# Kernel tuning notes

Hardware: AMD Instinct MI355X
Metric: run time of the kernel (lower is better)

Reference implementation:

```python
import jax, jax.numpy as jnp
import numpy as np

D_MODEL = 2048
N_HEAD = 16
HEAD_DIM = D_MODEL // N_HEAD
SCALE = 1.0 / (HEAD_DIM ** 0.5)


def setup_inputs() -> dict:
    key = jax.random.key(0)
    kx, kq, kk, kv, ko = jax.random.split(key, 5)
    std = 1.0 / np.sqrt(D_MODEL)
    return {
        "x": jax.random.normal(kx, (2, 2048, D_MODEL), dtype=jnp.float32),
        "w_q": jax.random.normal(kq, (D_MODEL, D_MODEL), dtype=jnp.float32) * std,
        "w_k": jax.random.normal(kk, (D_MODEL, D_MODEL), dtype=jnp.float32) * std,
        "w_v": jax.random.normal(kv, (D_MODEL, D_MODEL), dtype=jnp.float32) * std,
        "w_o": jax.random.normal(ko, (D_MODEL, D_MODEL), dtype=jnp.float32) * std,
    }


def reference(x, w_q, w_k, w_v, w_o):
    b, s, d = x.shape
    # nn.Linear(d,d,bias=False): y = x @ W^T, weights stored [out, in]
    def proj(w):
        y = jnp.einsum("bsd,ed->bse", x, w)
        return y.reshape(b, s, N_HEAD, HEAD_DIM).transpose(0, 2, 1, 3)  # [b,h,s,hd]
    q, k, v = proj(w_q), proj(w_k), proj(w_v)
    scores = jnp.einsum("bhqd,bhkd->bhqk", q, k) * SCALE  # [b,h,s,s]
    probs = jax.nn.softmax(scores, axis=-1)
    attn = jnp.einsum("bhqk,bhkd->bhqd", probs, v)
    attn = attn.transpose(0, 2, 1, 3).reshape(b, s, d)
    return jnp.einsum("bsd,ed->bse", attn, w_o)
```

## Files before the change

### kernel.cpp

```cpp
#include <hip/hip_runtime.h>

#define D_MODEL 2048
#define SEQ 2048
#define BATCH 2
#define NH 16
#define HD 128
#define MTOT (BATCH * SEQ)

static constexpr float SCALE_LOG2E = 0.08838834764831845f * 1.4426950408889634f;

typedef __bf16 bf16x8 __attribute__((ext_vector_type(8)));
typedef _Float16 f16x4 __attribute__((ext_vector_type(4)));
typedef float f32x4 __attribute__((ext_vector_type(4)));

__device__ inline unsigned short f2bf(float f) {
  unsigned int u = __builtin_bit_cast(unsigned int, f);
  u += 0x7fffu + ((u >> 16) & 1u);
  return (unsigned short)(u >> 16);
}

__device__ inline float fast_exp2(float x) {
#if __has_builtin(__builtin_amdgcn_exp2f)
  return __builtin_amdgcn_exp2f(x);
#else
  return exp2f(x);
#endif
}

__device__ inline void gload_lds16(const void* g, void* s) {
  __builtin_amdgcn_global_load_lds(
      (__attribute__((address_space(1))) void*)g,
      (__attribute__((address_space(3))) void*)s, 16, 0, 0);
}

__global__ __launch_bounds__(256) void cvt_bf16(const float* __restrict__ in,
                                                unsigned short* __restrict__ out,
                                                int n4) {
  int i = blockIdx.x * 256 + threadIdx.x;
  if (i < n4) {
    float4 v = ((const float4*)in)[i];
    ushort4 o;
    o.x = f2bf(v.x); o.y = f2bf(v.y); o.z = f2bf(v.z); o.w = f2bf(v.w);
    ((ushort4*)out)[i] = o;
  }
}

template <int OUT_BF16>
__global__ __launch_bounds__(256, 2) void gemm_bt(
    const unsigned short* __restrict__ A, const unsigned short* __restrict__ B,
    void* __restrict__ Cp, int M, int N, int K) {
  __shared__ __align__(16) unsigned short As[128 * 32];
  __shared__ __align__(16) unsigned short Bs[128 * 32];
  const int tid = threadIdx.x;
  const int lane = tid & 63;
  const int wave = tid >> 6;
  const int m0 = blockIdx.y * 128;
  const int n0 = blockIdx.x * 128;
  const int wm = (wave >> 1) * 64;
  const int wn = (wave & 1) * 64;

  const int c0 = wave * 2, c1 = wave * 2 + 1;
  const int sr0 = c0 * 16 + (lane >> 2);
  const int sr1 = c1 * 16 + (lane >> 2);
  const int sk = (lane & 3) * 8;
  const unsigned short* Ag0 = A + (size_t)(m0 + sr0) * K + sk;
  const unsigned short* Ag1 = A + (size_t)(m0 + sr1) * K + sk;
  const unsigned short* Bg0 = B + (size_t)(n0 + sr0) * K + sk;
  const unsigned short* Bg1 = B + (size_t)(n0 + sr1) * K + sk;
  unsigned short* lA0 = As + c0 * 512;
  unsigned short* lA1 = As + c1 * 512;
  unsigned short* lB0 = Bs + c0 * 512;
  unsigned short* lB1 = Bs + c1 * 512;

  f32x4 acc[4][4] = {};
  const int fm = lane & 15;
  const int fk = (lane >> 4) * 8;

  for (int k0 = 0; k0 < K; k0 += 32) {
    __syncthreads();
    gload_lds16(Ag0 + k0, lA0);
    gload_lds16(Ag1 + k0, lA1);
    gload_lds16(Bg0 + k0, lB0);
    gload_lds16(Bg1 + k0, lB1);
    __builtin_amdgcn_s_waitcnt(0);
    __syncthreads();
    bf16x8 a[4], b[4];
#pragma unroll
    for (int i = 0; i < 4; i++)
      a[i] = *(const bf16x8*)(As + (wm + i * 16 + fm) * 32 + fk);
#pragma unroll
    for (int j = 0; j < 4; j++)
      b[j] = *(const bf16x8*)(Bs + (wn + j * 16 + fm) * 32 + fk);
#pragma unroll
    for (int i = 0; i < 4; i++)
#pragma unroll
      for (int j = 0; j < 4; j++)
        acc[i][j] = __builtin_amdgcn_mfma_f32_16x16x32_bf16(a[i], b[j], acc[i][j], 0, 0, 0);
  }

  const int er = (lane >> 4) * 4;
  const int ec = lane & 15;
#pragma unroll
  for (int i = 0; i < 4; i++)
#pragma unroll
    for (int j = 0; j < 4; j++) {
      const int mm = m0 + wm + i * 16 + er;
      const int nn = n0 + wn + j * 16 + ec;
#pragma unroll
      for (int r = 0; r < 4; r++) {
        if (OUT_BF16)
          ((unsigned short*)Cp)[(size_t)(mm + r) * N + nn] = f2bf(acc[i][j][r]);
        else
          ((float*)Cp)[(size_t)(mm + r) * N + nn] = acc[i][j][r];
      }
    }
}

__global__ __launch_bounds__(256) void transpose_v(const unsigned short* __restrict__ V,
                                                   unsigned short* __restrict__ Vt) {
  __shared__ unsigned short t[64][72];
  const int bh = blockIdx.z, b = bh >> 4, h = bh & 15;
  const int s0 = blockIdx.x * 64, d0 = blockIdx.y * 64;
  const int rr = threadIdx.x >> 4;
  const int c4 = (threadIdx.x & 15) * 4;
#pragma unroll
  for (int i = 0; i < 4; i++) {
    int row = i * 16 + rr;
    ushort4 v = *(const ushort4*)(V + (size_t)(b * SEQ + s0 + row) * D_MODEL + h * HD + d0 + c4);
    t[row][c4] = v.x; t[row][c4 + 1] = v.y; t[row][c4 + 2] = v.z; t[row][c4 + 3] = v.w;
  }
  __syncthreads();
#pragma unroll
  for (int i = 0; i < 4; i++) {
    int drow = i * 16 + rr;
    ushort4 o;
#pragma unroll
    for (int e = 0; e < 4; e++) {
      unsigned int bits = (unsigned int)t[c4 + e][drow] << 16;
      _Float16 hv = (_Float16)__builtin_bit_cast(float, bits);
      ((unsigned short*)&o)[e] = __builtin_bit_cast(unsigned short, hv);
    }
    *(ushort4*)(Vt + ((size_t)bh * HD + d0 + drow) * SEQ + s0 + c4) = o;
  }
}

__global__ __launch_bounds__(256, 2) void flash_attn(
    const unsigned short* __restrict__ Q, const unsigned short* __restrict__ Kg,
    const unsigned short* __restrict__ Vt, unsigned short* __restrict__ Og) {
  __shared__ __align__(16) unsigned short Ks[2][64 * 128];
  __shared__ __align__(16) unsigned short Vs[2][128 * 64];
  const int tid = threadIdx.x;
  const int lane = tid & 63;
  const int wave = tid >> 6;
  const int quad = lane >> 4;
  const int l15 = lane & 15;
  const int bh = blockIdx.y;
  const int b = bh >> 4, h = bh & 15;
  const int q0 = blockIdx.x * 128;

  const size_t kbase = (size_t)(b * SEQ) * D_MODEL + h * HD;
  const size_t vbase = (size_t)bh * HD * SEQ;

  bf16x8 qf[2][4];
#pragma unroll
  for (int t = 0; t < 2; t++)
#pragma unroll
    for (int kc = 0; kc < 4; kc++)
      qf[t][kc] = *(const bf16x8*)(Q + (size_t)(b * SEQ + q0 + wave * 32 + t * 16 + l15) * D_MODEL +
                                   h * HD + kc * 32 + quad * 8);

  const unsigned short* kg[4];
  const unsigned short* vg[4];
  int klofs[4], vlofs[4];
#pragma unroll
  for (int i = 0; i < 4; i++) {
    int krow = wave * 16 + i * 4 + quad;
    int kc_ = l15 ^ (i * 4 + quad);
    kg[i] = Kg + kbase + (size_t)krow * D_MODEL + kc_ * 8;
    klofs[i] = (wave * 16 + i * 4) * 128;
    int vrow = wave * 32 + i * 8 + (lane >> 3);
    int vc_ = (lane & 7) ^ (lane >> 3);
    vg[i] = Vt + vbase + (size_t)vrow * SEQ + vc_ * 8;
    vlofs[i] = (wave * 32 + i * 8) * 64;
  }

#pragma unroll
  for (int i = 0; i < 4; i++) gload_lds16(kg[i], &Ks[0][klofs[i]]);
#pragma unroll
  for (int i = 0; i < 4; i++) gload_lds16(vg[i], &Vs[0][vlofs[i]]);
#pragma unroll
  for (int i = 0; i < 4; i++) { kg[i] += 64 * D_MODEL; vg[i] += 64; }
  __builtin_amdgcn_s_waitcnt(0);
  __syncthreads();

  float lsum[2] = {0.f, 0.f};
  f32x4 Oa[2][8] = {};

  for (int it = 0; it < SEQ / 64; ++it) {
    const int cur = it & 1;
    if (it < SEQ / 64 - 1) {
#pragma unroll
      for (int i = 0; i < 4; i++) gload_lds16(kg[i], &Ks[cur ^ 1][klofs[i]]);
#pragma unroll
      for (int i = 0; i < 4; i++) gload_lds16(vg[i], &Vs[cur ^ 1][vlofs[i]]);
#pragma unroll
      for (int i = 0; i < 4; i++) { kg[i] += 64 * D_MODEL; vg[i] += 64; }
    }

    const unsigned short* kb = &Ks[cur][0];
    f32x4 sacc[2][4] = {};
#pragma unroll
    for (int js = 0; js < 4; js++)
#pragma unroll
      for (int kc = 0; kc < 4; kc++) {
        bf16x8 kf = *(const bf16x8*)(kb + (js * 16 + l15) * 128 + (((kc * 4 + quad) ^ l15) * 8));
        sacc[0][js] = __builtin_amdgcn_mfma_f32_16x16x32_bf16(kf, qf[0][kc], sacc[0][js], 0, 0, 0);
        sacc[1][js] = __builtin_amdgcn_mfma_f32_16x16x32_bf16(kf, qf[1][kc], sacc[1][js], 0, 0, 0);
      }

    f16x4 pb[2][4];
#pragma unroll
    for (int t = 0; t < 2; t++)
#pragma unroll
      for (int js = 0; js < 4; js++)
#pragma unroll
        for (int r = 0; r < 4; r++) {
          float p = fast_exp2(sacc[t][js][r] * SCALE_LOG2E);
          lsum[t] += p;
          pb[t][js][r] = (_Float16)p;
        }

    const unsigned short* vb_ = &Vs[cur][0];
#pragma unroll
    for (int jt = 0; jt < 8; jt++)
#pragma unroll
      for (int js = 0; js < 4; js++) {
        f16x4 vf = *(const f16x4*)(vb_ + (jt * 16 + l15) * 64 +
                                   (((js * 2 + (quad >> 1)) ^ (lane & 7)) * 8) + (quad & 1) * 4);
        Oa[0][jt] = __builtin_amdgcn_mfma_f32_16x16x16f16(vf, pb[0][js], Oa[0][jt], 0, 0, 0);
        Oa[1][jt] = __builtin_amdgcn_mfma_f32_16x16x16f16(vf, pb[1][js], Oa[1][jt], 0, 0, 0);
      }

    __builtin_amdgcn_s_waitcnt(0);
    __syncthreads();
  }

  float inv[2];
#pragma unroll
  for (int t = 0; t < 2; t++) {
    float s = lsum[t];
    s += __shfl_xor(s, 16);
    s += __shfl_xor(s, 32);
    inv[t] = 1.0f / s;
  }

#pragma unroll
  for (int t = 0; t < 2; t++) {
    const size_t rowbase = (size_t)(b * SEQ + q0 + wave * 32 + t * 16 + l15) * D_MODEL + h * HD;
#pragma unroll
    for (int jt = 0; jt < 8; jt++) {
      ushort4 o;
      o.x = f2bf(Oa[t][jt][0] * inv[t]);
      o.y = f2bf(Oa[t][jt][1] * inv[t]);
      o.z = f2bf(Oa[t][jt][2] * inv[t]);
      o.w = f2bf(Oa[t][jt][3] * inv[t]);
      *(ushort4*)(Og + rowbase + jt * 16 + quad * 4) = o;
    }
  }
}

extern "C" void kernel_launch(void* const* d_in, const int* in_sizes, int n_in,
                              void* d_out, int out_size, void* d_ws, size_t ws_size,
                              hipStream_t stream) {
  const float* x = (const float*)d_in[0];
  const float* wq = (const float*)d_in[1];
  const float* wk = (const float*)d_in[2];
  const float* wv = (const float*)d_in[3];
  const float* wo = (const float*)d_in[4];
  float* out = (float*)d_out;
  char* ws = (char*)d_ws;
  const size_t MB = 1u << 20;
  if (ws_size < 112 * MB) return;

  unsigned short* xb = (unsigned short*)(ws);
  unsigned short* wqb = (unsigned short*)(ws + 16 * MB);
  unsigned short* wkb = (unsigned short*)(ws + 24 * MB);
  unsigned short* wvb = (unsigned short*)(ws + 32 * MB);
  unsigned short* wob = (unsigned short*)(ws + 40 * MB);
  unsigned short* Qb = (unsigned short*)(ws + 48 * MB);
  unsigned short* Kb = (unsigned short*)(ws + 64 * MB);
  unsigned short* Vb = (unsigned short*)(ws + 80 * MB);
  unsigned short* Vtb = (unsigned short*)(ws + 96 * MB);
  unsigned short* Ab = xb;

  cvt_bf16<<<8192, 256, 0, stream>>>(x, xb, (MTOT * D_MODEL) / 4);
  cvt_bf16<<<4096, 256, 0, stream>>>(wq, wqb, (D_MODEL * D_MODEL) / 4);
  cvt_bf16<<<4096, 256, 0, stream>>>(wk, wkb, (D_MODEL * D_MODEL) / 4);
  cvt_bf16<<<4096, 256, 0, stream>>>(wv, wvb, (D_MODEL * D_MODEL) / 4);
  cvt_bf16<<<4096, 256, 0, stream>>>(wo, wob, (D_MODEL * D_MODEL) / 4);

  dim3 gg(D_MODEL / 128, MTOT / 128);
  gemm_bt<1><<<gg, 256, 0, stream>>>(xb, wqb, Qb, MTOT, D_MODEL, D_MODEL);
  gemm_bt<1><<<gg, 256, 0, stream>>>(xb, wkb, Kb, MTOT, D_MODEL, D_MODEL);
  gemm_bt<1><<<gg, 256, 0, stream>>>(xb, wvb, Vb, MTOT, D_MODEL, D_MODEL);

  transpose_v<<<dim3(SEQ / 64, HD / 64, BATCH * NH), 256, 0, stream>>>(Vb, Vtb);

  flash_attn<<<dim3(SEQ / 128, BATCH * NH), 256, 0, stream>>>(Qb, Kb, Vtb, Ab);

  gemm_bt<0><<<gg, 256, 0, stream>>>(Ab, wob, out, MTOT, D_MODEL, D_MODEL);
}
```

Baseline: 433.4 us.

## Fuse QKV projections into one GEMM with in-epilogue V transpose

Merges the five conversion launches into one multi-slice kernel and the three projection GEMMs into a single GEMM over concatenated Q/K/V weights. Q and K go to an interleaved buffer with row stride 4096. V tiles are transposed through shared memory in the epilogue and written directly as fp16 Vt, which removes the separate transpose kernel and its extra round trip to memory. The attention grid is also remapped so blocks sharing a batch-head are spread across the ID space, which may change cache locality. The cost is larger LDS use in the QKV GEMM and a wider tail wave for the cvt launch, since the weight slices have idle blocks.

```diff
diff --git a/kernel.cpp b/kernel.cpp
--- a/kernel.cpp
+++ b/kernel.cpp
@@ -5,7 +5,9 @@
 #define BATCH 2
 #define NH 16
 #define HD 128
-#define MTOT (BATCH * SEQ)
+#define MTOT 4096
+#define NQKV 6144
+#define QSTRIDE 4096
 
 static constexpr float SCALE_LOG2E = 0.08838834764831845f * 1.4426950408889634f;
 
@@ -33,27 +35,46 @@
       (__attribute__((address_space(3))) void*)s, 16, 0, 0);
 }
 
-__global__ __launch_bounds__(256) void cvt_bf16(const float* __restrict__ in,
-                                                unsigned short* __restrict__ out,
-                                                int n4) {
+__global__ __launch_bounds__(256) void cvt_all(
+    const float* __restrict__ x, const float* __restrict__ wq,
+    const float* __restrict__ wk, const float* __restrict__ wv,
+    const float* __restrict__ wo, unsigned short* __restrict__ xb,
+    unsigned short* __restrict__ wqkv, unsigned short* __restrict__ wob) {
+  const int y = blockIdx.y;
+  const float* src;
+  unsigned short* dst;
+  int n4;
+  if (y == 0) { src = x; dst = xb; n4 = MTOT * D_MODEL / 4; }
+  else if (y == 4) { src = wo; dst = wob; n4 = D_MODEL * D_MODEL / 4; }
+  else {
+    src = (y == 1) ? wq : (y == 2) ? wk : wv;
+    dst = wqkv + (size_t)(y - 1) * D_MODEL * D_MODEL;
+    n4 = D_MODEL * D_MODEL / 4;
+  }
   int i = blockIdx.x * 256 + threadIdx.x;
   if (i < n4) {
-    float4 v = ((const float4*)in)[i];
+    float4 v = ((const float4*)src)[i];
     ushort4 o;
     o.x = f2bf(v.x); o.y = f2bf(v.y); o.z = f2bf(v.z); o.w = f2bf(v.w);
-    ((ushort4*)out)[i] = o;
-  }
-}
-
-template <int OUT_BF16>
-__global__ __launch_bounds__(256, 2) void gemm_bt(
+    ((ushort4*)dst)[i] = o;
+  }
+}
+
+__global__ __launch_bounds__(256, 2) void gemm_qkv(
     const unsigned short* __restrict__ A, const unsigned short* __restrict__ B,
-    void* __restrict__ Cp, int M, int N, int K) {
-  __shared__ __align__(16) unsigned short As[128 * 32];
-  __shared__ __align__(16) unsigned short Bs[128 * 32];
+    unsigned short* __restrict__ QK, unsigned short* __restrict__ Vt) {
+  __shared__ __align__(16) union {
+    struct { unsigned short As[128 * 32]; unsigned short Bs[128 * 32]; } s;
+    unsigned short T[128 * 136];
+  } u;
+  unsigned short* As = u.s.As;
+  unsigned short* Bs = u.s.Bs;
+  const int K = D_MODEL;
   const int tid = threadIdx.x;
   const int lane = tid & 63;
   const int wave = tid >> 6;
+  const int quad = lane >> 4;
+  const int l15 = lane & 15;
   const int m0 = blockIdx.y * 128;
   const int n0 = blockIdx.x * 128;
   const int wm = (wave >> 1) * 64;
@@ -73,8 +94,8 @@
   unsigned short* lB1 = Bs + c1 * 512;
 
   f32x4 acc[4][4] = {};
-  const int fm = lane & 15;
-  const int fk = (lane >> 4) * 8;
+  const int fm = l15;
+  const int fk = quad * 8;
 
   for (int k0 = 0; k0 < K; k0 += 32) {
     __syncthreads();
@@ -98,6 +119,100 @@
         acc[i][j] = __builtin_amdgcn_mfma_f32_16x16x32_bf16(a[i], b[j], acc[i][j], 0, 0, 0);
   }
 
+  const int er = quad * 4;
+  const int ec = l15;
+  if (n0 < 4096) {
+#pragma unroll
+    for (int i = 0; i < 4; i++)
+#pragma unroll
+      for (int j = 0; j < 4; j++) {
+        const int mm = m0 + wm + i * 16 + er;
+        const int nn = n0 + wn + j * 16 + ec;
+#pragma unroll
+        for (int r = 0; r < 4; r++)
+          QK[(size_t)(mm + r) * QSTRIDE + nn] = f2bf(acc[i][j][r]);
+      }
+  } else {
+    __syncthreads();
+    const int vcol0 = n0 - 4096;
+    const int h = vcol0 >> 7;
+    const int b = m0 >> 11;
+    const int bh = b * NH + h;
+    const int sbase = m0 & (SEQ - 1);
+#pragma unroll
+    for (int i = 0; i < 4; i++)
+#pragma unroll
+      for (int j = 0; j < 4; j++) {
+        const int dl = wn + j * 16 + ec;
+        const int sl = wm + i * 16 + er;
+        f16x4 hv;
+#pragma unroll
+        for (int r = 0; r < 4; r++) hv[r] = (_Float16)acc[i][j][r];
+        *(f16x4*)(u.T + dl * 136 + sl) = hv;
+      }
+    __syncthreads();
+#pragma unroll
+    for (int p = 0; p < 8; p++) {
+      const int d = p * 16 + (tid >> 4);
+      const int s = (tid & 15) * 8;
+      float4 chunk = *(const float4*)(u.T + d * 136 + s);
+      *(float4*)(Vt + ((size_t)(bh * HD + d)) * SEQ + sbase + s) = chunk;
+    }
+  }
+}
+
+__global__ __launch_bounds__(256, 2) void gemm_out(
+    const unsigned short* __restrict__ A, const unsigned short* __restrict__ B,
+    float* __restrict__ C, int M, int N, int K) {
+  __shared__ __align__(16) unsigned short As[128 * 32];
+  __shared__ __align__(16) unsigned short Bs[128 * 32];
+  const int tid = threadIdx.x;
+  const int lane = tid & 63;
+  const int wave = tid >> 6;
+  const int m0 = blockIdx.y * 128;
+  const int n0 = blockIdx.x * 128;
+  const int wm = (wave >> 1) * 64;
+  const int wn = (wave & 1) * 64;
+
+  const int c0 = wave * 2, c1 = wave * 2 + 1;
+  const int sr0 = c0 * 16 + (lane >> 2);
+  const int sr1 = c1 * 16 + (lane >> 2);
+  const int sk = (lane & 3) * 8;
+  const unsigned short* Ag0 = A + (size_t)(m0 + sr0) * K + sk;
+  const unsigned short* Ag1 = A + (size_t)(m0 + sr1) * K + sk;
+  const unsigned short* Bg0 = B + (size_t)(n0 + sr0) * K + sk;
+  const unsigned short* Bg1 = B + (size_t)(n0 + sr1) * K + sk;
+  unsigned short* lA0 = As + c0 * 512;
+  unsigned short* lA1 = As + c1 * 512;
+  unsigned short* lB0 = Bs + c0 * 512;
+  unsigned short* lB1 = Bs + c1 * 512;
+
+  f32x4 acc[4][4] = {};
+  const int fm = lane & 15;
+  const int fk = (lane >> 4) * 8;
+
+  for (int k0 = 0; k0 < K; k0 += 32) {
+    __syncthreads();
+    gload_lds16(Ag0 + k0, lA0);
+    gload_lds16(Ag1 + k0, lA1);
+    gload_lds16(Bg0 + k0, lB0);
+    gload_lds16(Bg1 + k0, lB1);
+    __builtin_amdgcn_s_waitcnt(0);
+    __syncthreads();
+    bf16x8 a[4], b[4];
+#pragma unroll
+    for (int i = 0; i < 4; i++)
+      a[i] = *(const bf16x8*)(As + (wm + i * 16 + fm) * 32 + fk);
+#pragma unroll
+    for (int j = 0; j < 4; j++)
+      b[j] = *(const bf16x8*)(Bs + (wn + j * 16 + fm) * 32 + fk);
+#pragma unroll
+    for (int i = 0; i < 4; i++)
+#pragma unroll
+      for (int j = 0; j < 4; j++)
+        acc[i][j] = __builtin_amdgcn_mfma_f32_16x16x32_bf16(a[i], b[j], acc[i][j], 0, 0, 0);
+  }
+
   const int er = (lane >> 4) * 4;
   const int ec = lane & 15;
 #pragma unroll
@@ -107,46 +222,14 @@
       const int mm = m0 + wm + i * 16 + er;
       const int nn = n0 + wn + j * 16 + ec;
 #pragma unroll
-      for (int r = 0; r < 4; r++) {
-        if (OUT_BF16)
-          ((unsigned short*)Cp)[(size_t)(mm + r) * N + nn] = f2bf(acc[i][j][r]);
-        else
-          ((float*)Cp)[(size_t)(mm + r) * N + nn] = acc[i][j][r];
-      }
+      for (int r = 0; r < 4; r++)
+        C[(size_t)(mm + r) * N + nn] = acc[i][j][r];
     }
 }
 
-__global__ __launch_bounds__(256) void transpose_v(const unsigned short* __restrict__ V,
-                                                   unsigned short* __restrict__ Vt) {
-  __shared__ unsigned short t[64][72];
-  const int bh = blockIdx.z, b = bh >> 4, h = bh & 15;
-  const int s0 = blockIdx.x * 64, d0 = blockIdx.y * 64;
-  const int rr = threadIdx.x >> 4;
-  const int c4 = (threadIdx.x & 15) * 4;
-#pragma unroll
-  for (int i = 0; i < 4; i++) {
-    int row = i * 16 + rr;
-    ushort4 v = *(const ushort4*)(V + (size_t)(b * SEQ + s0 + row) * D_MODEL + h * HD + d0 + c4);
-    t[row][c4] = v.x; t[row][c4 + 1] = v.y; t[row][c4 + 2] = v.z; t[row][c4 + 3] = v.w;
-  }
-  __syncthreads();
-#pragma unroll
-  for (int i = 0; i < 4; i++) {
-    int drow = i * 16 + rr;
-    ushort4 o;
-#pragma unroll
-    for (int e = 0; e < 4; e++) {
-      unsigned int bits = (unsigned int)t[c4 + e][drow] << 16;
-      _Float16 hv = (_Float16)__builtin_bit_cast(float, bits);
-      ((unsigned short*)&o)[e] = __builtin_bit_cast(unsigned short, hv);
-    }
-    *(ushort4*)(Vt + ((size_t)bh * HD + d0 + drow) * SEQ + s0 + c4) = o;
-  }
-}
-
 __global__ __launch_bounds__(256, 2) void flash_attn(
-    const unsigned short* __restrict__ Q, const unsigned short* __restrict__ Kg,
-    const unsigned short* __restrict__ Vt, unsigned short* __restrict__ Og) {
+    const unsigned short* __restrict__ QK, const unsigned short* __restrict__ Vt,
+    unsigned short* __restrict__ Og) {
   __shared__ __align__(16) unsigned short Ks[2][64 * 128];
   __shared__ __align__(16) unsigned short Vs[2][128 * 64];
   const int tid = threadIdx.x;
@@ -154,11 +237,14 @@
   const int wave = tid >> 6;
   const int quad = lane >> 4;
   const int l15 = lane & 15;
-  const int bh = blockIdx.y;
+  const int id = blockIdx.x;
+  const int xr = id & 7;
+  const int kk = id >> 3;
+  const int bh = xr * 4 + (kk >> 4);
   const int b = bh >> 4, h = bh & 15;
-  const int q0 = blockIdx.x * 128;
-
-  const size_t kbase = (size_t)(b * SEQ) * D_MODEL + h * HD;
+  const int q0 = (kk & 15) * 128;
+
+  const size_t kbase = (size_t)(b * SEQ) * QSTRIDE + D_MODEL + h * HD;
   const size_t vbase = (size_t)bh * HD * SEQ;
 
   bf16x8 qf[2][4];
@@ -166,7 +252,7 @@
   for (int t = 0; t < 2; t++)
 #pragma unroll
     for (int kc = 0; kc < 4; kc++)
-      qf[t][kc] = *(const bf16x8*)(Q + (size_t)(b * SEQ + q0 + wave * 32 + t * 16 + l15) * D_MODEL +
+      qf[t][kc] = *(const bf16x8*)(QK + (size_t)(b * SEQ + q0 + wave * 32 + t * 16 + l15) * QSTRIDE +
                                    h * HD + kc * 32 + quad * 8);
 
   const unsigned short* kg[4];
@@ -176,7 +262,7 @@
   for (int i = 0; i < 4; i++) {
     int krow = wave * 16 + i * 4 + quad;
     int kc_ = l15 ^ (i * 4 + quad);
-    kg[i] = Kg + kbase + (size_t)krow * D_MODEL + kc_ * 8;
+    kg[i] = QK + kbase + (size_t)krow * QSTRIDE + kc_ * 8;
     klofs[i] = (wave * 16 + i * 4) * 128;
     int vrow = wave * 32 + i * 8 + (lane >> 3);
     int vc_ = (lane & 7) ^ (lane >> 3);
@@ -189,7 +275,7 @@
 #pragma unroll
   for (int i = 0; i < 4; i++) gload_lds16(vg[i], &Vs[0][vlofs[i]]);
 #pragma unroll
-  for (int i = 0; i < 4; i++) { kg[i] += 64 * D_MODEL; vg[i] += 64; }
+  for (int i = 0; i < 4; i++) { kg[i] += 64 * QSTRIDE; vg[i] += 64; }
   __builtin_amdgcn_s_waitcnt(0);
   __syncthreads();
 
@@ -204,7 +290,7 @@
 #pragma unroll
       for (int i = 0; i < 4; i++) gload_lds16(vg[i], &Vs[cur ^ 1][vlofs[i]]);
 #pragma unroll
-      for (int i = 0; i < 4; i++) { kg[i] += 64 * D_MODEL; vg[i] += 64; }
+      for (int i = 0; i < 4; i++) { kg[i] += 64 * QSTRIDE; vg[i] += 64; }
     }
 
     const unsigned short* kb = &Ks[cur][0];
@@ -280,33 +366,20 @@
   float* out = (float*)d_out;
   char* ws = (char*)d_ws;
   const size_t MB = 1u << 20;
-  if (ws_size < 112 * MB) return;
+  if (ws_size < 96 * MB) return;
 
   unsigned short* xb = (unsigned short*)(ws);
-  unsigned short* wqb = (unsigned short*)(ws + 16 * MB);
-  unsigned short* wkb = (unsigned short*)(ws + 24 * MB);
-  unsigned short* wvb = (unsigned short*)(ws + 32 * MB);
+  unsigned short* wqkv = (unsigned short*)(ws + 16 * MB);
   unsigned short* wob = (unsigned short*)(ws + 40 * MB);
-  unsigned short* Qb = (unsigned short*)(ws + 48 * MB);
-  unsigned short* Kb = (unsigned short*)(ws + 64 * MB);
-  unsigned short* Vb = (unsigned short*)(ws + 80 * MB);
-  unsigned short* Vtb = (unsigned short*)(ws + 96 * MB);
+  unsigned short* QKb = (unsigned short*)(ws + 48 * MB);
+  unsigned short* Vtb = (unsigned short*)(ws + 80 * MB);
   unsigned short* Ab = xb;
 
-  cvt_bf16<<<8192, 256, 0, stream>>>(x, xb, (MTOT * D_MODEL) / 4);
-  cvt_bf16<<<4096, 256, 0, stream>>>(wq, wqb, (D_MODEL * D_MODEL) / 4);
-  cvt_bf16<<<4096, 256, 0, stream>>>(wk, wkb, (D_MODEL * D_MODEL) / 4);
-  cvt_bf16<<<4096, 256, 0, stream>>>(wv, wvb, (D_MODEL * D_MODEL) / 4);
-  cvt_bf16<<<4096, 256, 0, stream>>>(wo, wob, (D_MODEL * D_MODEL) / 4);
-
-  dim3 gg(D_MODEL / 128, MTOT / 128);
-  gemm_bt<1><<<gg, 256, 0, stream>>>(xb, wqb, Qb, MTOT, D_MODEL, D_MODEL);
-  gemm_bt<1><<<gg, 256, 0, stream>>>(xb, wkb, Kb, MTOT, D_MODEL, D_MODEL);
-  gemm_bt<1><<<gg, 256, 0, stream>>>(xb, wvb, Vb, MTOT, D_MODEL, D_MODEL);
-
-  transpose_v<<<dim3(SEQ / 64, HD / 64, BATCH * NH), 256, 0, stream>>>(Vb, Vtb);
-
-  flash_attn<<<dim3(SEQ / 128, BATCH * NH), 256, 0, stream>>>(Qb, Kb, Vtb, Ab);
-
-  gemm_bt<0><<<gg, 256, 0, stream>>>(Ab, wob, out, MTOT, D_MODEL, D_MODEL);
-}
+  cvt_all<<<dim3(8192, 5), 256, 0, stream>>>(x, wq, wk, wv, wo, xb, wqkv, wob);
+
+  gemm_qkv<<<dim3(NQKV / 128, MTOT / 128), 256, 0, stream>>>(xb, wqkv, QKb, Vtb);
+
+  flash_attn<<<512, 256, 0, stream>>>(QKb, Vtb, Ab);
+
+  gemm_out<<<dim3(D_MODEL / 128, MTOT / 128), 256, 0, stream>>>(Ab, wob, out, MTOT, D_MODEL, D_MODEL);
+}
```

Measured after the change: 394.3 us. -9.0%, faster.
